# Performance work log

Measured on AMD Instinct MI355X. Metric: run time of the kernel, lower is better.

## Reference

```python
import jax, jax.numpy as jnp
import numpy as np


def _gcn_norm(edge_index, num_nodes):
    """Add self-loops and compute symmetric normalization coeffs (PyG GCNConv default)."""
    loop = jnp.arange(num_nodes, dtype=edge_index.dtype)
    row = jnp.concatenate([edge_index[0], loop])  # source nodes
    col = jnp.concatenate([edge_index[1], loop])  # target nodes
    deg = jax.ops.segment_sum(jnp.ones_like(col, dtype=jnp.float32), col,
                              num_segments=num_nodes)
    dinv = jnp.where(deg > 0, jax.lax.rsqrt(deg), 0.0)
    norm = dinv[row] * dinv[col]  # [E + N]
    return row, col, norm


def _gcn_conv(x, W, b, row, col, norm, num_nodes):
    xw = x @ W                                   # [N, out]
    msg = xw[row] * norm[:, None]                # gather + scale, [E+N, out]
    out = jax.ops.segment_sum(msg, col, num_segments=num_nodes)  # scatter-add
    return out + b


def setup_inputs() -> dict:
    key = jax.random.key(0)
    ks = jax.random.split(key, 12)
    N, E, F, H, C, G = 100000, 1600000, 64, 64, 10, 128
    x = jax.random.normal(ks[0], (N, F), dtype=jnp.float32)
    edge_index = jax.random.randint(ks[1], (2, E), 0, N, dtype=jnp.int64)
    batch = jnp.sort(jax.random.randint(ks[2], (N,), 0, G, dtype=jnp.int64))
    def glorot(k, fan_in, fan_out):
        s = jnp.sqrt(6.0 / (fan_in + fan_out))
        return jax.random.uniform(k, (fan_in, fan_out), jnp.float32, -s, s)
    return {
        "x": x, "edge_index": edge_index, "batch": batch, "num_graphs": G,
        "W0": glorot(ks[3], F, H), "b0": jnp.zeros((H,), jnp.float32),
        "W1": glorot(ks[4], H, H), "b1": jnp.zeros((H,), jnp.float32),
        "W2": glorot(ks[5], H, H), "b2": jnp.zeros((H,), jnp.float32),
        "Wro": glorot(ks[6], H, C), "bro": jnp.zeros((C,), jnp.float32),
    }


def reference(x, edge_index, batch, num_graphs, W0, b0, W1, b1, W2, b2, Wro, bro):
    N = x.shape[0]
    row, col, norm = _gcn_norm(edge_index, N)
    for W, b in ((W0, b0), (W1, b1), (W2, b2)):
        x = jax.nn.silu(_gcn_conv(x, W, b, row, col, norm, N))
        # dropout p=0.0 / eval mode -> identity
    # global_mean_pool over batch ids
    sums = jax.ops.segment_sum(x, batch, num_segments=num_graphs)   # [G, H]
    cnts = jax.ops.segment_sum(jnp.ones((N,), x.dtype), batch, num_segments=num_graphs)
    pooled = sums / jnp.maximum(cnts, 1.0)[:, None]
    # readout: Linear + ReLU (make_mlp with hidden_layers=1), then log_softmax
    logits = jax.nn.relu(pooled @ Wro + bro)
    return jax.nn.log_softmax(logits, axis=1)
```

## Files before the change

### kernel.cpp

```cpp
#include <hip/hip_runtime.h>
#include <hip/hip_fp16.h>


#define CH 256
#define BSH 7
#define BNODES 128

typedef _Float16 half8 __attribute__((ext_vector_type(8)));
typedef float float4v __attribute__((ext_vector_type(4)));

__global__ void k_wt(const float* __restrict__ W0, const float* __restrict__ W1,
                     const float* __restrict__ W2, __half* __restrict__ Wt) {
    const float* Ws[3] = {W0, W1, W2};
    const float* W = Ws[blockIdx.x];
    __half* out = Wt + blockIdx.x * 4096;
    for (int idx = threadIdx.x; idx < 4096; idx += 256) {
        int k = idx >> 6, feat = idx & 63;
        int ks = k >> 5, kg = (k >> 3) & 3, j = k & 7;
        int ct = feat >> 4, c16 = feat & 15;
        out[((ct * 2 + ks) * 4 + kg) * 128 + c16 * 8 + j] = __float2half_rn(W[k * 64 + feat]);
    }
}

__global__ __launch_bounds__(256) void k_hist(const int* __restrict__ col, int E, int Ec, int NB,
                                              int* __restrict__ histG) {
    __shared__ int h[1024];
    int c = blockIdx.x, tid = threadIdx.x;
    for (int i = tid; i < NB; i += 256) h[i] = 0;
    __syncthreads();
    int lo = c * Ec, hi = min(E, lo + Ec);
    for (int e = lo + tid; e < hi; e += 256) atomicAdd(&h[col[e] >> BSH], 1);
    __syncthreads();
    for (int i = tid; i < NB; i += 256) histG[c * NB + i] = h[i];
}

__global__ void k_scanb(int* __restrict__ histG, int NB, int* __restrict__ btot) {
    int b = blockIdx.x;
    int l = threadIdx.x;
    int v[4], p[4];
#pragma unroll
    for (int k = 0; k < 4; ++k) { v[k] = histG[(k * 64 + l) * NB + b]; p[k] = v[k]; }
    for (int off = 1; off < 64; off <<= 1) {
#pragma unroll
        for (int k = 0; k < 4; ++k) {
            int t = __shfl_up(p[k], off);
            if (l >= off) p[k] += t;
        }
    }
    int acc = 0;
#pragma unroll
    for (int k = 0; k < 4; ++k) {
        int tot = __shfl(p[k], 63);
        histG[(k * 64 + l) * NB + b] = acc + p[k] - v[k];
        acc += tot;
    }
    if (l == 0) btot[b] = acc;
}

__global__ void k_scant(const int* __restrict__ btot, int NB, int E, int* __restrict__ bstart,
                        float* __restrict__ sums, int GF) {
    __shared__ int s[1024];
    int tid = threadIdx.x;
    for (int i = tid; i < GF; i += 1024) sums[i] = 0.f;
    int v = (tid < NB) ? btot[tid] : 0;
    s[tid] = v;
    __syncthreads();
    for (int off = 1; off < 1024; off <<= 1) {
        int t = (tid >= off) ? s[tid - off] : 0;
        __syncthreads();
        s[tid] += t;
        __syncthreads();
    }
    if (tid < NB) bstart[tid] = s[tid] - v;
    if (tid == 0) bstart[NB] = E;
}

__global__ __launch_bounds__(1024) void k_scatter(const int* __restrict__ col, const int* __restrict__ row,
                                                  int E, int Ec, int NB,
                                                  const int* __restrict__ histG,
                                                  const int* __restrict__ bstart,
                                                  unsigned int* __restrict__ edges) {
    __shared__ int cur[1024];
    int c = blockIdx.x, tid = threadIdx.x;
    for (int i = tid; i < NB; i += 1024) cur[i] = bstart[i] + histG[c * NB + i];
    __syncthreads();
    int lo = c * Ec, hi = min(E, lo + Ec);
    for (int e = lo + tid; e < hi; e += 1024) {
        int cc = col[e];
        int b = cc >> BSH;
        int pos = atomicAdd(&cur[b], 1);
        edges[pos] = (unsigned int)row[e] | ((unsigned int)(cc & (BNODES - 1)) << 25);
    }
}

__global__ __launch_bounds__(512) void k_sort2(const unsigned int* __restrict__ edges,
                                               const int* __restrict__ bstart, int N, int E, int NB,
                                               int* __restrict__ srcs, int* __restrict__ starts,
                                               float* __restrict__ dinv) {
    __shared__ int cnt[BNODES];
    __shared__ int cur[BNODES];
    int b = blockIdx.x, tid = threadIdx.x;
    if (tid < BNODES) cnt[tid] = 0;
    __syncthreads();
    int lo = bstart[b], hi = bstart[b + 1];
    for (int e = lo + tid; e < hi; e += 512) atomicAdd(&cnt[edges[e] >> 25], 1);
    __syncthreads();
    if (tid < 64) {
        int v0 = cnt[tid], v1 = cnt[64 + tid];
        int p0 = v0, p1 = v1;
        for (int off = 1; off < 64; off <<= 1) {
            int t0 = __shfl_up(p0, off);
            int t1 = __shfl_up(p1, off);
            if (tid >= off) { p0 += t0; p1 += t1; }
        }
        int A = __shfl(p0, 63);
        cur[tid] = lo + p0 - v0;
        cur[64 + tid] = lo + A + p1 - v1;
    }
    __syncthreads();
    int ng = b * BNODES + tid;
    if (tid < BNODES && ng < N) {
        starts[ng] = cur[tid];
        dinv[ng] = rsqrtf((float)cnt[tid] + 1.0f);
    }
    if (b == 0 && tid == 0) starts[N] = E;
    __syncthreads();
    for (int e = lo + tid; e < hi; e += 512) {
        unsigned int p = edges[e];
        int pos = atomicAdd(&cur[p >> 25], 1);
        srcs[pos] = (int)((p & 0x1FFFFFFu) << 3);
    }
}

template <int IN_HALF>
__global__ __launch_bounds__(256) void k_gemm(const void* __restrict__ xin,
                                              const __half* __restrict__ Wt,
                                              const float* __restrict__ dinv,
                                              __half* __restrict__ yh, int N) {
    int tid = threadIdx.x;
    int lane = tid & 63, wv = tid >> 6;
    int c16 = lane & 15, kg = lane >> 4;
    const _Float16* wt = (const _Float16*)Wt;
    half8 bf[4][2];
#pragma unroll
    for (int ct = 0; ct < 4; ++ct)
#pragma unroll
        for (int ks = 0; ks < 2; ++ks)
            bf[ct][ks] = *(const half8*)(wt + ((ct * 2 + ks) * 4 + kg) * 128 + c16 * 8);

    int tiles = (N + 15) >> 4;
    for (int t = blockIdx.x * 4 + wv; t < tiles; t += gridDim.x * 4) {
        int base = t << 4;
        int arow = base + c16;
        bool valid = arow < N;
        half8 af0, af1;
        if (valid) {
            if (IN_HALF) {
                const __half* xh = (const __half*)xin;
                af0 = *(const half8*)(xh + (size_t)arow * 64 + kg * 8);
                af1 = *(const half8*)(xh + (size_t)arow * 64 + 32 + kg * 8);
            } else {
                const float* xf = (const float*)xin;
                float4 u0 = *(const float4*)(xf + (size_t)arow * 64 + kg * 8);
                float4 u1 = *(const float4*)(xf + (size_t)arow * 64 + kg * 8 + 4);
                float4 u2 = *(const float4*)(xf + (size_t)arow * 64 + 32 + kg * 8);
                float4 u3 = *(const float4*)(xf + (size_t)arow * 64 + 32 + kg * 8 + 4);
                af0[0]=(_Float16)u0.x; af0[1]=(_Float16)u0.y; af0[2]=(_Float16)u0.z; af0[3]=(_Float16)u0.w;
                af0[4]=(_Float16)u1.x; af0[5]=(_Float16)u1.y; af0[6]=(_Float16)u1.z; af0[7]=(_Float16)u1.w;
                af1[0]=(_Float16)u2.x; af1[1]=(_Float16)u2.y; af1[2]=(_Float16)u2.z; af1[3]=(_Float16)u2.w;
                af1[4]=(_Float16)u3.x; af1[5]=(_Float16)u3.y; af1[6]=(_Float16)u3.z; af1[7]=(_Float16)u3.w;
            }
        } else {
#pragma unroll
            for (int j = 0; j < 8; ++j) { af0[j] = (_Float16)0.f; af1[j] = (_Float16)0.f; }
        }
        float d = valid ? dinv[arow] : 0.f;
#pragma unroll
        for (int ct = 0; ct < 4; ++ct) {
            float4v c = {0.f, 0.f, 0.f, 0.f};
            c = __builtin_amdgcn_mfma_f32_16x16x32_f16(bf[ct][0], af0, c, 0, 0, 0);
            c = __builtin_amdgcn_mfma_f32_16x16x32_f16(bf[ct][1], af1, c, 0, 0, 0);
            if (valid) {
                float2 st;
                __half2* hp = (__half2*)&st;
                hp[0] = __float22half2_rn(make_float2(c[0] * d, c[1] * d));
                hp[1] = __float22half2_rn(make_float2(c[2] * d, c[3] * d));
                *(float2*)(yh + (size_t)arow * 64 + ct * 16 + kg * 4) = st;
            }
        }
    }
}

__global__ __launch_bounds__(256) void k_agg(const int* __restrict__ starts,
                                             const int* __restrict__ srcs,
                                             const __half* __restrict__ yh,
                                             const float* __restrict__ dinv,
                                             const float* __restrict__ b,
                                             __half* __restrict__ xh, int N) {
    int wv = (blockIdx.x * blockDim.x + threadIdx.x) >> 6;
    int lane = threadIdx.x & 63;
    int g = lane >> 3, i = lane & 7;
    int node = wv * 8 + g;
    bool valid = node < N;
    const float4* y4 = (const float4*)yh;
    __half2 a0, a1, a2, a3;
    a0 = a1 = a2 = a3 = __half2half2(__ushort_as_half((unsigned short)0));
    int s = 0, t = 0;
    if (valid) {
        s = starts[node]; t = starts[node + 1];
        float4 raw = y4[(size_t)node * 8 + i];
        const __half2* h = (const __half2*)&raw;
        a0 = h[0]; a1 = h[1]; a2 = h[2]; a3 = h[3];
    }
    int e = s;
    for (; e + 7 < t; e += 8) {
        float4 r[8];
#pragma unroll
        for (int k = 0; k < 8; ++k) r[k] = y4[(size_t)srcs[e + k] + i];
#pragma unroll
        for (int k = 0; k < 8; ++k) {
            const __half2* h = (const __half2*)&r[k];
            a0 = __hadd2(a0, h[0]); a1 = __hadd2(a1, h[1]);
            a2 = __hadd2(a2, h[2]); a3 = __hadd2(a3, h[3]);
        }
    }
    for (; e + 3 < t; e += 4) {
        float4 r[4];
#pragma unroll
        for (int k = 0; k < 4; ++k) r[k] = y4[(size_t)srcs[e + k] + i];
#pragma unroll
        for (int k = 0; k < 4; ++k) {
            const __half2* h = (const __half2*)&r[k];
            a0 = __hadd2(a0, h[0]); a1 = __hadd2(a1, h[1]);
            a2 = __hadd2(a2, h[2]); a3 = __hadd2(a3, h[3]);
        }
    }
    for (; e < t; ++e) {
        float4 r0 = y4[(size_t)srcs[e] + i];
        const __half2* h0 = (const __half2*)&r0;
        a0 = __hadd2(a0, h0[0]); a1 = __hadd2(a1, h0[1]);
        a2 = __hadd2(a2, h0[2]); a3 = __hadd2(a3, h0[3]);
    }
    if (valid) {
        float d = dinv[node];
        float4 b0 = ((const float4*)b)[2 * i];
        float4 b1 = ((const float4*)b)[2 * i + 1];
        float bb[8] = {b0.x, b0.y, b0.z, b0.w, b1.x, b1.y, b1.z, b1.w};
        float2 f0 = __half22float2(a0), f1 = __half22float2(a1);
        float2 f2 = __half22float2(a2), f3 = __half22float2(a3);
        float sums[8] = {f0.x, f0.y, f1.x, f1.y, f2.x, f2.y, f3.x, f3.y};
        float o[8];
#pragma unroll
        for (int f = 0; f < 8; ++f) {
            float v = d * sums[f] + bb[f];
            o[f] = v / (1.f + __expf(-v));
        }
        float4 outv;
        __half2* oh = (__half2*)&outv;
#pragma unroll
        for (int p = 0; p < 4; ++p) oh[p] = __float22half2_rn(make_float2(o[2 * p], o[2 * p + 1]));
        ((float4*)xh)[(size_t)node * 8 + i] = outv;
    }
}

__global__ __launch_bounds__(256) void k_pool1(const __half* __restrict__ xh,
                                               const int* __restrict__ batch, int N, int chunk,
                                               float* __restrict__ sums) {
    int wvg = blockIdx.x * 4 + (threadIdx.x >> 6);
    int lane = threadIdx.x & 63;
    int lo = wvg * chunk;
    int hi = min(N, lo + chunk);
    if (lo >= hi) return;
    float acc = 0.f;
    int gcur = batch[lo];
    for (int n = lo; n < hi; ++n) {
        int gn = batch[n];
        if (gn != gcur) {
            atomicAdd(&sums[gcur * 64 + lane], acc);
            acc = 0.f;
            gcur = gn;
        }
        acc += __half2float(xh[(size_t)n * 64 + lane]);
    }
    atomicAdd(&sums[gcur * 64 + lane], acc);
}

__global__ void k_readout(const float* __restrict__ sums, const int* __restrict__ batch, int N,
                          const float* __restrict__ Wro, const float* __restrict__ bro,
                          float* __restrict__ out, int C) {
    int g = blockIdx.x;
    int j = threadIdx.x;
    __shared__ float sp[64];
    __shared__ float sl[32];
    int lo = 0, hb = N;
    while (lo < hb) { int m = (lo + hb) >> 1; if (batch[m] < g) lo = m + 1; else hb = m; }
    int lo2 = lo, hi2 = N;
    while (lo2 < hi2) { int m = (lo2 + hi2) >> 1; if (batch[m] < g + 1) lo2 = m + 1; else hi2 = m; }
    float cnt = fmaxf((float)(hi2 - lo), 1.0f);
    sp[j] = sums[g * 64 + j] / cnt;
    __syncthreads();
    if (j < C) {
        float a = bro[j];
        for (int k = 0; k < 64; ++k) a += sp[k] * Wro[k * C + j];
        sl[j] = fmaxf(a, 0.f);
    }
    __syncthreads();
    if (j == 0) {
        float m = -1e30f;
        for (int c = 0; c < C; ++c) m = fmaxf(m, sl[c]);
        float sum = 0.f;
        for (int c = 0; c < C; ++c) sum += __expf(sl[c] - m);
        float lse = m + __logf(sum);
        for (int c = 0; c < C; ++c) out[g * C + c] = sl[c] - lse;
    }
}

static inline size_t align256(size_t v) { return (v + 255) & ~(size_t)255; }

extern "C" void kernel_launch(void* const* d_in, const int* in_sizes, int n_in,
                              void* d_out, int out_size, void* d_ws, size_t ws_size,
                              hipStream_t stream) {
    const float* x    = (const float*)d_in[0];
    const int*   ei   = (const int*)d_in[1];
    const int*   batch= (const int*)d_in[2];
    const float* W[3] = {(const float*)d_in[4], (const float*)d_in[6], (const float*)d_in[8]};
    const float* b[3] = {(const float*)d_in[5], (const float*)d_in[7], (const float*)d_in[9]};
    const float* Wro  = (const float*)d_in[10];
    const float* bro  = (const float*)d_in[11];

    int N = in_sizes[2];
    int E = in_sizes[1] / 2;
    int C = in_sizes[10] / 64;
    int G = out_size / C;

    const int* row = ei;
    const int* col = ei + E;

    int NB = (N + BNODES - 1) >> BSH;
    int Ec = (E + CH - 1) / CH;

    char* ws = (char*)d_ws;
    size_t off = 0;
    float* dinv    = (float*)(ws + off);        off = align256(off + (size_t)N * 4);
    int*   histG   = (int*)(ws + off);          off = align256(off + (size_t)CH * NB * 4);
    int*   btot    = (int*)(ws + off);          off = align256(off + (size_t)NB * 4);
    int*   bstart  = (int*)(ws + off);          off = align256(off + (size_t)(NB + 1) * 4);
    unsigned int* edges  = (unsigned int*)(ws + off); off = align256(off + (size_t)E * 4);
    int*   srcs    = (int*)(ws + off);          off = align256(off + (size_t)E * 4);
    int*   starts  = (int*)(ws + off);          off = align256(off + (size_t)(N + 1) * 4);
    __half* yh     = (__half*)(ws + off);       off = align256(off + (size_t)N * 64 * 2);
    __half* xh     = (__half*)(ws + off);       off = align256(off + (size_t)N * 64 * 2);
    float* sums    = (float*)(ws + off);        off = align256(off + (size_t)G * 64 * 4);
    __half* Wt     = (__half*)(ws + off);       off = align256(off + (size_t)3 * 4096 * 2);

    k_wt<<<3, 256, 0, stream>>>(W[0], W[1], W[2], Wt);
    k_hist<<<CH, 256, 0, stream>>>(col, E, Ec, NB, histG);
    k_scanb<<<NB, 64, 0, stream>>>(histG, NB, btot);
    k_scant<<<1, 1024, 0, stream>>>(btot, NB, E, bstart, sums, G * 64);
    k_scatter<<<CH, 1024, 0, stream>>>(col, row, E, Ec, NB, histG, bstart, edges);
    k_sort2<<<NB, 512, 0, stream>>>(edges, bstart, N, E, NB, srcs, starts, dinv);

    int aggB = (N + 31) / 32;
    int gemmB = 1568;

    k_gemm<0><<<gemmB, 256, 0, stream>>>(x, Wt, dinv, yh, N);
    k_agg<<<aggB, 256, 0, stream>>>(starts, srcs, yh, dinv, b[0], xh, N);
    k_gemm<1><<<gemmB, 256, 0, stream>>>(xh, Wt + 4096, dinv, yh, N);
    k_agg<<<aggB, 256, 0, stream>>>(starts, srcs, yh, dinv, b[1], xh, N);
    k_gemm<1><<<gemmB, 256, 0, stream>>>(xh, Wt + 8192, dinv, yh, N);
    k_agg<<<aggB, 256, 0, stream>>>(starts, srcs, yh, dinv, b[2], xh, N);

    int nwaves = 4096;
    int chunk = (N + nwaves - 1) / nwaves;
    k_pool1<<<nwaves / 4, 256, 0, stream>>>(xh, batch, N, chunk, sums);
    k_readout<<<G, 64, 0, stream>>>(sums, batch, N, Wro, bro, (float*)d_out, C);
}
```

Baseline: 200.2 us.

## Reorder nodes by in-degree within each bucket to balance aggregation waves

In the bucket sort kernel, builds a per-bucket histogram of node in-degrees and counting-sorts the 128 nodes of each bucket by degree into a permutation array. The aggregation kernel then processes nodes in that permuted order, so the 8 nodes sharing a wavefront have similar edge counts and less divergence in the per-edge loop. This adds an indirection load per node and scatters the output writes within a bucket, plus some extra shared-memory scan work in the sort.

```diff
diff --git a/kernel.cpp b/kernel.cpp
--- a/kernel.cpp
+++ b/kernel.cpp
@@ -96,15 +96,19 @@
 __global__ __launch_bounds__(512) void k_sort2(const unsigned int* __restrict__ edges,
                                                const int* __restrict__ bstart, int N, int E, int NB,
                                                int* __restrict__ srcs, int* __restrict__ starts,
-                                               float* __restrict__ dinv) {
+                                               float* __restrict__ dinv, int* __restrict__ perm) {
     __shared__ int cnt[BNODES];
     __shared__ int cur[BNODES];
+    __shared__ int dh[256];
     int b = blockIdx.x, tid = threadIdx.x;
     if (tid < BNODES) cnt[tid] = 0;
+    if (tid < 256) dh[tid] = 0;
     __syncthreads();
     int lo = bstart[b], hi = bstart[b + 1];
     for (int e = lo + tid; e < hi; e += 512) atomicAdd(&cnt[edges[e] >> 25], 1);
     __syncthreads();
+    int ng = b * BNODES + tid;
+    if (tid < BNODES && ng < N) atomicAdd(&dh[min(cnt[tid], 255)], 1);
     if (tid < 64) {
         int v0 = cnt[tid], v1 = cnt[64 + tid];
         int p0 = v0, p1 = v1;
@@ -118,13 +122,35 @@
         cur[64 + tid] = lo + A + p1 - v1;
     }
     __syncthreads();
-    int ng = b * BNODES + tid;
     if (tid < BNODES && ng < N) {
         starts[ng] = cur[tid];
         dinv[ng] = rsqrtf((float)cnt[tid] + 1.0f);
     }
     if (b == 0 && tid == 0) starts[N] = E;
-    __syncthreads();
+    if (tid < 64) {
+        int v[4], pp[4];
+#pragma unroll
+        for (int k = 0; k < 4; ++k) { v[k] = dh[k * 64 + tid]; pp[k] = v[k]; }
+        for (int off = 1; off < 64; off <<= 1) {
+#pragma unroll
+            for (int k = 0; k < 4; ++k) {
+                int t2 = __shfl_up(pp[k], off);
+                if (tid >= off) pp[k] += t2;
+            }
+        }
+        int acc = 0;
+#pragma unroll
+        for (int k = 0; k < 4; ++k) {
+            int tot = __shfl(pp[k], 63);
+            dh[k * 64 + tid] = acc + pp[k] - v[k];
+            acc += tot;
+        }
+    }
+    __syncthreads();
+    if (tid < BNODES && ng < N) {
+        int r = atomicAdd(&dh[min(cnt[tid], 255)], 1);
+        perm[b * BNODES + r] = ng;
+    }
     for (int e = lo + tid; e < hi; e += 512) {
         unsigned int p = edges[e];
         int pos = atomicAdd(&cur[p >> 25], 1);
@@ -193,6 +219,7 @@
 
 __global__ __launch_bounds__(256) void k_agg(const int* __restrict__ starts,
                                              const int* __restrict__ srcs,
+                                             const int* __restrict__ perm,
                                              const __half* __restrict__ yh,
                                              const float* __restrict__ dinv,
                                              const float* __restrict__ b,
@@ -200,13 +227,15 @@
     int wv = (blockIdx.x * blockDim.x + threadIdx.x) >> 6;
     int lane = threadIdx.x & 63;
     int g = lane >> 3, i = lane & 7;
-    int node = wv * 8 + g;
-    bool valid = node < N;
+    int p = wv * 8 + g;
+    bool valid = p < N;
+    int node = 0;
     const float4* y4 = (const float4*)yh;
     __half2 a0, a1, a2, a3;
     a0 = a1 = a2 = a3 = __half2half2(__ushort_as_half((unsigned short)0));
     int s = 0, t = 0;
     if (valid) {
+        node = perm[p];
         s = starts[node]; t = starts[node + 1];
         float4 raw = y4[(size_t)node * 8 + i];
         const __half2* h = (const __half2*)&raw;
@@ -258,7 +287,7 @@
         float4 outv;
         __half2* oh = (__half2*)&outv;
 #pragma unroll
-        for (int p = 0; p < 4; ++p) oh[p] = __float22half2_rn(make_float2(o[2 * p], o[2 * p + 1]));
+        for (int q = 0; q < 4; ++q) oh[q] = __float22half2_rn(make_float2(o[2 * q], o[2 * q + 1]));
         ((float4*)xh)[(size_t)node * 8 + i] = outv;
     }
 }
@@ -348,6 +377,7 @@
     unsigned int* edges  = (unsigned int*)(ws + off); off = align256(off + (size_t)E * 4);
     int*   srcs    = (int*)(ws + off);          off = align256(off + (size_t)E * 4);
     int*   starts  = (int*)(ws + off);          off = align256(off + (size_t)(N + 1) * 4);
+    int*   perm    = (int*)(ws + off);          off = align256(off + (size_t)N * 4);
     __half* yh     = (__half*)(ws + off);       off = align256(off + (size_t)N * 64 * 2);
     __half* xh     = (__half*)(ws + off);       off = align256(off + (size_t)N * 64 * 2);
     float* sums    = (float*)(ws + off);        off = align256(off + (size_t)G * 64 * 4);
@@ -358,17 +388,17 @@
     k_scanb<<<NB, 64, 0, stream>>>(histG, NB, btot);
     k_scant<<<1, 1024, 0, stream>>>(btot, NB, E, bstart, sums, G * 64);
     k_scatter<<<CH, 1024, 0, stream>>>(col, row, E, Ec, NB, histG, bstart, edges);
-    k_sort2<<<NB, 512, 0, stream>>>(edges, bstart, N, E, NB, srcs, starts, dinv);
+    k_sort2<<<NB, 512, 0, stream>>>(edges, bstart, N, E, NB, srcs, starts, dinv, perm);
 
     int aggB = (N + 31) / 32;
     int gemmB = 1568;
 
     k_gemm<0><<<gemmB, 256, 0, stream>>>(x, Wt, dinv, yh, N);
-    k_agg<<<aggB, 256, 0, stream>>>(starts, srcs, yh, dinv, b[0], xh, N);
+    k_agg<<<aggB, 256, 0, stream>>>(starts, srcs, perm, yh, dinv, b[0], xh, N);
     k_gemm<1><<<gemmB, 256, 0, stream>>>(xh, Wt + 4096, dinv, yh, N);
-    k_agg<<<aggB, 256, 0, stream>>>(starts, srcs, yh, dinv, b[1], xh, N);
+    k_agg<<<aggB, 256, 0, stream>>>(starts, srcs, perm, yh, dinv, b[1], xh, N);
     k_gemm<1><<<gemmB, 256, 0, stream>>>(xh, Wt + 8192, dinv, yh, N);
-    k_agg<<<aggB, 256, 0, stream>>>(starts, srcs, yh, dinv, b[2], xh, N);
+    k_agg<<<aggB, 256, 0, stream>>>(starts, srcs, perm, yh, dinv, b[2], xh, N);
 
     int nwaves = 4096;
     int chunk = (N + nwaves - 1) / nwaves;
```

New measurement: 218.4 us. +9.1%, slower.
